# Kernel tuning notes

Measured on AMD Instinct MI355X. Metric: run time of the kernel, lower is better.

Reference implementation:

```python
import jax, jax.numpy as jnp
import numpy as np

B, S, N = 1, 8, 512
DV, DM = 256, 64
INNER, H, WS = 256, 8, 3
DH = INNER // H


def setup_inputs() -> dict:
    key = jax.random.key(0)
    ks = jax.random.split(key, 7)
    w = lambda k, shape: jax.random.normal(k, shape, dtype=jnp.float32) * 0.02
    return {
        "values": jax.random.normal(ks[0], (B, S, N, DV), dtype=jnp.float32),
        "metadata": jax.random.normal(ks[1], (B, S, N, DM), dtype=jnp.float32),
        "w_meta_outer": w(ks[2], (DM, 2 * INNER)),   # meta_to_qk of outer block
        "w_qkv": w(ks[3], (DV, 3 * INNER)),           # values_to_qkv (no bias)
        "w_meta_inner": w(ks[4], (DM, 2 * INNER)),   # meta_to_qk of inner block
        "w_out": w(ks[5], (INNER, DV)),               # output_proj Linear weight
        "b_out": jnp.zeros((DV,), dtype=jnp.float32), # output_proj Linear bias
    }


def _forward(values, metadata, w_meta_outer, w_qkv, w_meta_inner, w_out, b_out):
    # ---- outer: source-level metadata attention to pick top-WS windows ----
    meta_mean = metadata.mean(axis=2)                      # [B,S,DM]
    qm, km = jnp.split(meta_mean @ w_meta_outer, 2, axis=-1)
    qm = jnp.clip(qm, -5, 5)
    km = jnp.clip(km, -5, 5)
    dots = jnp.einsum('bqd,bkd->bqk', qm, km) * (INNER ** -0.5)
    meta_attn = jax.nn.softmax(dots, axis=-1) + 2.0 * jnp.eye(S, dtype=dots.dtype)
    _, top_idx = jax.lax.top_k(meta_attn, WS)              # [B,S,WS], sorted desc

    # ---- gather adaptive windows over the source axis ----
    bidx = jnp.arange(B)[:, None, None]
    win_vals = values[bidx, top_idx]                       # [B,S,WS,N,DV]
    win_meta = metadata[bidx, top_idx]                     # [B,S,WS,N,DM]

    # Keys/values over all WS*N window tokens; queries only for slot-0 tokens
    # (the original computes all queries then slices x[:,:,0]; softmax is
    # per-query so restricting queries gives identical math).
    kv_vals = win_vals.reshape(B * S, WS * N, DV)
    kv_meta = win_meta.reshape(B * S, WS * N, DM)
    q_vals = win_vals[:, :, 0].reshape(B * S, N, DV)
    q_meta = win_meta[:, :, 0].reshape(B * S, N, DM)

    # ---- inner: fused QpKp^T + QmKm^T attention ----
    qp = q_vals @ w_qkv[:, :INNER]
    kp = kv_vals @ w_qkv[:, INNER:2 * INNER]
    v = kv_vals @ w_qkv[:, 2 * INNER:]
    qm2 = q_meta @ w_meta_inner[:, :INNER]
    km2 = kv_meta @ w_meta_inner[:, INNER:]

    def heads(x):  # [bs, n, inner] -> [bs, H, n, DH]
        return x.reshape(x.shape[0], x.shape[1], H, DH).transpose(0, 2, 1, 3)

    qp, kp, v, qm2, km2 = map(heads, (qp, kp, v, qm2, km2))
    scale = DH ** -0.5
    scores = jnp.einsum('bhqd,bhkd->bhqk', jnp.clip(qp, -5, 5), jnp.clip(kp, -5, 5)) * scale
    scores = scores + jnp.einsum('bhqd,bhkd->bhqk', jnp.clip(qm2, -5, 5), jnp.clip(km2, -5, 5)) * scale
    attn = jax.nn.softmax(scores, axis=-1)                 # [B*S,H,N,WS*N]
    out = jnp.einsum('bhqk,bhkd->bhqd', attn, v)           # [B*S,H,N,DH]
    out = out.transpose(0, 2, 1, 3).reshape(B * S, N, INNER)
    out = out @ w_out + b_out                              # dropout=0 (eval)
    return out.reshape(B, S, N, DV)


def reference(values, metadata, w_meta_outer, w_qkv, w_meta_inner, w_out, b_out):
    return _forward(values, metadata, w_meta_outer, w_qkv, w_meta_inner, w_out, b_out)
```

## Files before the change

### kernel.cpp

```cpp
#include <hip/hip_runtime.h>
#include <hip/hip_bf16.h>

#define S_ 8
#define N_ 512
#define DV_ 256
#define DM_ 64
#define INNER_ 256
#define H_ 8
#define WS_ 3
#define DH_ 32

typedef __attribute__((ext_vector_type(8))) __bf16 bf16x8;
typedef __attribute__((ext_vector_type(4))) float f32x4;

__device__ __forceinline__ float clip5(float x) {
    return fminf(5.0f, fmaxf(-5.0f, x));
}
__device__ __forceinline__ unsigned short f2bf(float x) {
    __hip_bfloat16 h = __float2bfloat16(x);
    return *reinterpret_cast<unsigned short*>(&h);
}

__global__ __launch_bounds__(256) void prep(
    const float* __restrict__ w_qkv, const float* __restrict__ w_meta_inner,
    const float* __restrict__ w_out, const float* __restrict__ metadata,
    unsigned short* __restrict__ WqkvT, unsigned short* __restrict__ WmetaT,
    unsigned short* __restrict__ WoutT, float* __restrict__ mm_part)
{
    __shared__ float Tf[64][65];
    int b = blockIdx.x, tid = threadIdx.x;
    if (b < 72) {
        const float* src; unsigned short* dst; int Nsrc, Ktot, k0, n0;
        if (b < 48)      { src = w_qkv;        dst = WqkvT; Nsrc = 768; Ktot = 256; k0 = (b & 3) * 64; n0 = (b >> 2) * 64; }
        else if (b < 56) { src = w_meta_inner; dst = WmetaT; Nsrc = 512; Ktot = 64;  k0 = 0;            n0 = (b - 48) * 64; }
        else             { int t = b - 56; src = w_out; dst = WoutT; Nsrc = 256; Ktot = 256; k0 = (t & 3) * 64; n0 = (t >> 2) * 64; }
#pragma unroll
        for (int p = 0; p < 16; p++) {
            int i = p * 256 + tid; int r = i >> 6, cc = i & 63;
            Tf[r][cc] = src[(size_t)(k0 + r) * Nsrc + n0 + cc];
        }
        __syncthreads();
#pragma unroll
        for (int p = 0; p < 16; p++) {
            int i = p * 256 + tid; int r = i >> 6, cc = i & 63;
            dst[(size_t)(n0 + r) * Ktot + k0 + cc] = f2bf(Tf[cc][r]);
        }
    } else {
        int bb = b - 72;
        int s = bb >> 3, g = bb & 7;
        int d = tid & 63, t4 = tid >> 6;
        const float* base = metadata + ((size_t)(s * N_) + g * 64 + t4 * 16) * DM_ + d;
        float acc = 0.f;
#pragma unroll
        for (int i = 0; i < 16; i++) acc += base[(size_t)i * DM_];
        float* red = &Tf[0][0];
        red[tid] = acc;
        __syncthreads();
        if (tid < 64)
            mm_part[(size_t)bb * 64 + tid] =
                red[tid] + red[tid + 64] + red[tid + 128] + red[tid + 192];
    }
}

template<int ROLE>
__device__ __forceinline__ void gemm_body(
    unsigned short* smem,
    const float* __restrict__ A, const unsigned short* __restrict__ Bt,
    unsigned short* __restrict__ Qc, unsigned short* __restrict__ Kc,
    unsigned short* __restrict__ Vt,
    int m0, int n0g, int tid)
{
    constexpr int K = (ROLE == 1) ? 64 : 256;
    constexpr int KP = K + 8;
    unsigned short* As = smem;
    unsigned short* Bs = smem + 64 * KP;

    for (int i = tid; i < 64 * (K / 4); i += 256) {
        int r = i / (K / 4), g = i % (K / 4);
        float4 x = *(const float4*)(A + (size_t)(m0 + r) * K + 4 * g);
        *(ushort4*)&As[r * KP + 4 * g] =
            make_ushort4(f2bf(x.x), f2bf(x.y), f2bf(x.z), f2bf(x.w));
    }
    for (int i = tid; i < 64 * (K / 8); i += 256) {
        int r = i / (K / 8), g = i % (K / 8);
        *(bf16x8*)&Bs[r * KP + 8 * g] =
            *(const bf16x8*)(Bt + (size_t)(n0g + r) * K + 8 * g);
    }
    __syncthreads();

    const int w = tid >> 6, lane = tid & 63, c = lane & 15, qd = lane >> 4;
    const int mb = (w >> 1) * 32, nb = (w & 1) * 32;
    f32x4 acc[2][2];
    const f32x4 z = {0.f, 0.f, 0.f, 0.f};
#pragma unroll
    for (int mt = 0; mt < 2; mt++)
#pragma unroll
        for (int nt = 0; nt < 2; nt++) acc[mt][nt] = z;

#pragma unroll
    for (int kk = 0; kk < K / 32; kk++) {
        bf16x8 a[2], bb[2];
#pragma unroll
        for (int mt = 0; mt < 2; mt++)
            a[mt] = *(const bf16x8*)&As[(mb + mt * 16 + c) * KP + kk * 32 + qd * 8];
#pragma unroll
        for (int nt = 0; nt < 2; nt++)
            bb[nt] = *(const bf16x8*)&Bs[(nb + nt * 16 + c) * KP + kk * 32 + qd * 8];
#pragma unroll
        for (int mt = 0; mt < 2; mt++)
#pragma unroll
            for (int nt = 0; nt < 2; nt++)
                acc[mt][nt] = __builtin_amdgcn_mfma_f32_16x16x32_bf16(
                    a[mt], bb[nt], acc[mt][nt], 0, 0, 0);
    }

#pragma unroll
    for (int mt = 0; mt < 2; mt++)
#pragma unroll
        for (int nt = 0; nt < 2; nt++)
#pragma unroll
            for (int r = 0; r < 4; r++) {
                int tok = m0 + mb + mt * 16 + qd * 4 + r;
                int n = n0g + nb + nt * 16 + c;
                float v = acc[mt][nt][r];
                if (ROLE == 0) {
                    if (n < 512) {
                        unsigned short* dst = (n < 256) ? Qc : Kc;
                        int p = n & 255;
                        dst[(size_t)tok * 512 + (p >> 5) * 64 + (p & 31)] = f2bf(clip5(v));
                    } else {
                        int vc = n - 512, h = vc >> 5, dh = vc & 31;
                        int s = tok >> 9, ntok = tok & 511;
                        Vt[(size_t)((s * 8 + h) * 32 + dh) * 512 + ntok] = f2bf(v);
                    }
                } else {
                    unsigned short* dst = (n < 256) ? Qc : Kc;
                    int p = n & 255;
                    dst[(size_t)tok * 512 + (p >> 5) * 64 + 32 + (p & 31)] = f2bf(clip5(v));
                }
            }
}

__global__ __launch_bounds__(256) void fused1(
    const float* __restrict__ values, const float* __restrict__ metadata,
    const unsigned short* __restrict__ WqkvT,
    const unsigned short* __restrict__ WmetaT,
    const float* __restrict__ mm_part, const float* __restrict__ w_meta_outer,
    unsigned short* __restrict__ Qc, unsigned short* __restrict__ Kc,
    unsigned short* __restrict__ Vt, int* __restrict__ topidx)
{
    __shared__ __align__(16) unsigned short smem[2 * 64 * 264];
    const int b = blockIdx.x, tid = threadIdx.x;

    if (b == 0) {
        float* mml  = (float*)smem;
        float* qmS  = mml + 512;
        float* kmS  = qmS + 2048;
        float* dots = kmS + 2048;
        for (int i = tid; i < 512; i += 256) {
            int s = i >> 6, d = i & 63;
            float acc = 0.f;
#pragma unroll
            for (int g = 0; g < 8; g++) acc += mm_part[(size_t)(s * 8 + g) * 64 + d];
            mml[i] = acc * (1.0f / (float)N_);
        }
        __syncthreads();
        for (int i = tid; i < S_ * 512; i += 256) {
            int s = i >> 9, c = i & 511;
            float acc = 0.0f;
            for (int k = 0; k < DM_; k++) acc += mml[s * 64 + k] * w_meta_outer[k * 512 + c];
            acc = clip5(acc);
            if (c < 256) qmS[s * 256 + c] = acc; else kmS[s * 256 + c - 256] = acc;
        }
        __syncthreads();
        if (tid < 64) {
            int qi = tid >> 3, ki = tid & 7;
            float acc = 0.0f;
            for (int j = 0; j < INNER_; j++) acc += qmS[qi * 256 + j] * kmS[ki * 256 + j];
            dots[qi * 8 + ki] = acc * 0.0625f;
        }
        __syncthreads();
        if (tid < S_) {
            int r = tid;
            float mx = -1e30f;
            for (int k = 0; k < S_; k++) mx = fmaxf(mx, dots[r * 8 + k]);
            float e[S_], sum = 0.0f;
            for (int k = 0; k < S_; k++) { e[k] = __expf(dots[r * 8 + k] - mx); sum += e[k]; }
            float vals[S_];
            for (int k = 0; k < S_; k++) vals[k] = e[k] / sum + (k == r ? 2.0f : 0.0f);
            bool used[S_];
            for (int k = 0; k < S_; k++) used[k] = false;
            for (int w = 0; w < WS_; w++) {
                float best = -1e30f; int bi = 0;
                for (int k = 0; k < S_; k++) {
                    if (!used[k] && vals[k] > best) { best = vals[k]; bi = k; }
                }
                used[bi] = true;
                topidx[r * WS_ + w] = bi;
            }
        }
    } else if (b <= 768) {
        int g = b - 1;
        gemm_body<0>(smem, values, WqkvT, Qc, Kc, Vt, (g & 63) * 64, (g >> 6) * 64, tid);
    } else {
        int g = b - 769;
        gemm_body<1>(smem, metadata, WmetaT, Qc, Kc, Vt, (g & 63) * 64, (g >> 6) * 64, tid);
    }
}

__global__ __launch_bounds__(256) void attn_mfma(
    const int* __restrict__ topidx,
    const unsigned short* __restrict__ Qc,
    const unsigned short* __restrict__ Kc,
    const unsigned short* __restrict__ Vt,
    unsigned short* __restrict__ AO)
{
    const int s   = blockIdx.x;
    const int h   = blockIdx.y;
    const int qt  = blockIdx.z;
    const int tid = threadIdx.x;
    const int w    = tid >> 6;
    const int lane = tid & 63;
    const int c    = lane & 15;
    const int qd   = lane >> 4;
    const float scale = 0.17677669529663687f;

    __shared__ __align__(16) unsigned short Pq[4][64][40];
    __shared__ __align__(16) float Of[4][32][66];
    __shared__ float Ml[4][2][64];

    const int src0 = topidx[s * WS_ + 0];
    const int srcs[3] = { topidx[s * WS_ + 0], topidx[s * WS_ + 1], topidx[s * WS_ + 2] };

    bf16x8 qf[4][2];
    {
        const unsigned short* qbase =
            Qc + (size_t)(src0 * N_ + qt * 64) * 512 + h * 64 + qd * 8;
#pragma unroll
        for (int qg = 0; qg < 4; qg++)
#pragma unroll
            for (int kc = 0; kc < 2; kc++)
                qf[qg][kc] = *reinterpret_cast<const bf16x8*>(
                    qbase + (size_t)(qg * 16 + c) * 512 + kc * 32);
    }

    f32x4 oacc[2][4];
    const f32x4 zero4 = {0.f, 0.f, 0.f, 0.f};
#pragma unroll
    for (int mg = 0; mg < 2; mg++)
#pragma unroll
        for (int qg = 0; qg < 4; qg++) oacc[mg][qg] = zero4;
    float mrun[4], lrun[4];
#pragma unroll
    for (int qg = 0; qg < 4; qg++) { mrun[qg] = -3.0e38f; lrun[qg] = 0.f; }

    for (int step = 0; step < 12; step++) {
        const int chunk = step * 4 + w;
        const int src = srcs[chunk >> 4];
        const int klocal = (chunk & 15) * 32;

        bf16x8 kf[2][2];
        const unsigned short* kbase =
            Kc + (size_t)(src * N_ + klocal) * 512 + h * 64 + qd * 8;
#pragma unroll
        for (int mg = 0; mg < 2; mg++)
#pragma unroll
            for (int kc = 0; kc < 2; kc++)
                kf[mg][kc] = *reinterpret_cast<const bf16x8*>(
                    kbase + (size_t)(mg * 16 + c) * 512 + kc * 32);

        bf16x8 vf[2];
        const unsigned short* vbase =
            Vt + (size_t)((src * H_ + h) * DH_) * N_ + klocal + qd * 8;
#pragma unroll
        for (int mg = 0; mg < 2; mg++)
            vf[mg] = *reinterpret_cast<const bf16x8*>(vbase + (size_t)(mg * 16 + c) * N_);

        f32x4 sacc[2][4];
#pragma unroll
        for (int mg = 0; mg < 2; mg++)
#pragma unroll
            for (int qg = 0; qg < 4; qg++) sacc[mg][qg] = zero4;
#pragma unroll
        for (int kc = 0; kc < 2; kc++)
#pragma unroll
            for (int mg = 0; mg < 2; mg++)
#pragma unroll
                for (int qg = 0; qg < 4; qg++)
                    sacc[mg][qg] = __builtin_amdgcn_mfma_f32_16x16x32_bf16(
                        kf[mg][kc], qf[qg][kc], sacc[mg][qg], 0, 0, 0);

#pragma unroll
        for (int qg = 0; qg < 4; qg++) {
            float mx = sacc[0][qg][0];
#pragma unroll
            for (int r = 1; r < 4; r++) mx = fmaxf(mx, sacc[0][qg][r]);
#pragma unroll
            for (int r = 0; r < 4; r++) mx = fmaxf(mx, sacc[1][qg][r]);
            mx = fmaxf(mx, __shfl_xor(mx, 16));
            mx = fmaxf(mx, __shfl_xor(mx, 32));
            float mnew = fmaxf(mrun[qg], mx);
            float alpha = __expf((mrun[qg] - mnew) * scale);
            float msc = mnew * scale;
            float ps = 0.f;
            unsigned short pb[2][4];
#pragma unroll
            for (int mg = 0; mg < 2; mg++)
#pragma unroll
                for (int r = 0; r < 4; r++) {
                    float p = __expf(__builtin_fmaf(sacc[mg][qg][r], scale, -msc));
                    ps += p;
                    pb[mg][r] = f2bf(p);
                }
            ps += __shfl_xor(ps, 16);
            ps += __shfl_xor(ps, 32);
            lrun[qg] = lrun[qg] * alpha + ps;
            mrun[qg] = mnew;
#pragma unroll
            for (int mg = 0; mg < 2; mg++)
#pragma unroll
                for (int r = 0; r < 4; r++) oacc[mg][qg][r] *= alpha;
#pragma unroll
            for (int mg = 0; mg < 2; mg++) {
                ushort4 u = make_ushort4(pb[mg][0], pb[mg][1], pb[mg][2], pb[mg][3]);
                *reinterpret_cast<ushort4*>(&Pq[w][qg * 16 + c][mg * 16 + qd * 4]) = u;
            }
        }

        bf16x8 pf[4];
#pragma unroll
        for (int qg = 0; qg < 4; qg++)
            pf[qg] = *reinterpret_cast<const bf16x8*>(&Pq[w][qg * 16 + c][qd * 8]);
#pragma unroll
        for (int mg = 0; mg < 2; mg++)
#pragma unroll
            for (int qg = 0; qg < 4; qg++)
                oacc[mg][qg] = __builtin_amdgcn_mfma_f32_16x16x32_bf16(
                    vf[mg], pf[qg], oacc[mg][qg], 0, 0, 0);
    }

    __syncthreads();
#pragma unroll
    for (int qg = 0; qg < 4; qg++) {
        if (qd == 0) {
            Ml[w][0][qg * 16 + c] = mrun[qg];
            Ml[w][1][qg * 16 + c] = lrun[qg];
        }
#pragma unroll
        for (int mg = 0; mg < 2; mg++)
#pragma unroll
            for (int r = 0; r < 4; r++)
                Of[w][mg * 16 + qd * 4 + r][qg * 16 + c] = oacc[mg][qg][r];
    }
    __syncthreads();

    {
        int q = tid & 63;
        int dh0 = (tid >> 6) * 8;
        float mw[4], cw[4];
#pragma unroll
        for (int v = 0; v < 4; v++) mw[v] = Ml[v][0][q];
        float M = fmaxf(fmaxf(mw[0], mw[1]), fmaxf(mw[2], mw[3]));
        float L = 0.f;
#pragma unroll
        for (int v = 0; v < 4; v++) {
            cw[v] = __expf((mw[v] - M) * scale);
            L += cw[v] * Ml[v][1][q];
        }
        float inv = 1.0f / L;
        unsigned short* aorow =
            AO + (size_t)(s * N_ + qt * 64 + q) * 256 + h * 32 + dh0;
        unsigned short ub[8];
#pragma unroll
        for (int j = 0; j < 8; j++) {
            int dh = dh0 + j;
            float o = cw[0] * Of[0][dh][q] + cw[1] * Of[1][dh][q]
                    + cw[2] * Of[2][dh][q] + cw[3] * Of[3][dh][q];
            ub[j] = f2bf(o * inv);
        }
        uint4 u;
        u.x = (unsigned)ub[0] | ((unsigned)ub[1] << 16);
        u.y = (unsigned)ub[2] | ((unsigned)ub[3] << 16);
        u.z = (unsigned)ub[4] | ((unsigned)ub[5] << 16);
        u.w = (unsigned)ub[6] | ((unsigned)ub[7] << 16);
        *reinterpret_cast<uint4*>(aorow) = u;
    }
}

__global__ __launch_bounds__(256) void gemm_out(
    const unsigned short* __restrict__ AO, const unsigned short* __restrict__ Bt,
    const float* __restrict__ bias, float* __restrict__ outp)
{
    constexpr int K = 256;
    constexpr int KP = K + 8;
    __shared__ __align__(16) unsigned short As[64 * KP];
    __shared__ __align__(16) unsigned short Bs[64 * KP];
    const int tid = threadIdx.x;
    const int m0 = blockIdx.x * 64;
    const int n0g = blockIdx.y * 64;

    for (int i = tid; i < 64 * (K / 8); i += 256) {
        int r = i / (K / 8), g = i % (K / 8);
        *(bf16x8*)&As[r * KP + 8 * g] =
            *(const bf16x8*)(AO + (size_t)(m0 + r) * K + 8 * g);
    }
    for (int i = tid; i < 64 * (K / 8); i += 256) {
        int r = i / (K / 8), g = i % (K / 8);
        *(bf16x8*)&Bs[r * KP + 8 * g] =
            *(const bf16x8*)(Bt + (size_t)(n0g + r) * K + 8 * g);
    }
    __syncthreads();

    const int w = tid >> 6, lane = tid & 63, c = lane & 15, qd = lane >> 4;
    const int mb = (w >> 1) * 32, nb = (w & 1) * 32;
    f32x4 acc[2][2];
    const f32x4 z = {0.f, 0.f, 0.f, 0.f};
#pragma unroll
    for (int mt = 0; mt < 2; mt++)
#pragma unroll
        for (int nt = 0; nt < 2; nt++) acc[mt][nt] = z;

#pragma unroll
    for (int kk = 0; kk < K / 32; kk++) {
        bf16x8 a[2], bb[2];
#pragma unroll
        for (int mt = 0; mt < 2; mt++)
            a[mt] = *(const bf16x8*)&As[(mb + mt * 16 + c) * KP + kk * 32 + qd * 8];
#pragma unroll
        for (int nt = 0; nt < 2; nt++)
            bb[nt] = *(const bf16x8*)&Bs[(nb + nt * 16 + c) * KP + kk * 32 + qd * 8];
#pragma unroll
        for (int mt = 0; mt < 2; mt++)
#pragma unroll
            for (int nt = 0; nt < 2; nt++)
                acc[mt][nt] = __builtin_amdgcn_mfma_f32_16x16x32_bf16(
                    a[mt], bb[nt], acc[mt][nt], 0, 0, 0);
    }

#pragma unroll
    for (int mt = 0; mt < 2; mt++)
#pragma unroll
        for (int nt = 0; nt < 2; nt++)
#pragma unroll
            for (int r = 0; r < 4; r++) {
                int tok = m0 + mb + mt * 16 + qd * 4 + r;
                int n = n0g + nb + nt * 16 + c;
                outp[(size_t)tok * 256 + n] = acc[mt][nt][r] + bias[n];
            }
}

extern "C" void kernel_launch(void* const* d_in, const int* in_sizes, int n_in,
                              void* d_out, int out_size, void* d_ws, size_t ws_size,
                              hipStream_t stream) {
    const float* values       = (const float*)d_in[0];
    const float* metadata     = (const float*)d_in[1];
    const float* w_meta_outer = (const float*)d_in[2];
    const float* w_qkv        = (const float*)d_in[3];
    const float* w_meta_inner = (const float*)d_in[4];
    const float* w_out        = (const float*)d_in[5];
    const float* b_out        = (const float*)d_in[6];
    float* out = (float*)d_out;

    char* ws = (char*)d_ws;
    int* topidx = (int*)ws;
    float* mm_part = (float*)(ws + 256);
    unsigned short* WqkvT  = (unsigned short*)(ws + 20480);
    unsigned short* WmetaT = WqkvT + (size_t)768 * 256;
    unsigned short* WoutT  = WmetaT + (size_t)512 * 64;
    unsigned short* Qc     = WoutT + (size_t)256 * 256;
    unsigned short* Kc     = Qc + (size_t)4096 * 512;
    unsigned short* Vt     = Kc + (size_t)4096 * 512;
    unsigned short* AO     = Vt + (size_t)8 * 8 * 32 * 512;

    prep<<<dim3(136), dim3(256), 0, stream>>>(
        w_qkv, w_meta_inner, w_out, metadata, WqkvT, WmetaT, WoutT, mm_part);
    fused1<<<dim3(1281), dim3(256), 0, stream>>>(
        values, metadata, WqkvT, WmetaT, mm_part, w_meta_outer, Qc, Kc, Vt, topidx);
    attn_mfma<<<dim3(8, 8, 8), dim3(256), 0, stream>>>(topidx, Qc, Kc, Vt, AO);
    gemm_out<<<dim3(64, 4), dim3(256), 0, stream>>>(AO, WoutT, b_out, out);
}
```

Measured before the change: 124.4 us.

## Merge four kernels into one persistent cooperative kernel with grid syncs

Replaces the four separate launches (weight prep, QKV projection, attention, output GEMM) with a single cooperative persistent kernel. Each phase loops over its original work units with a grid-stride loop and is separated from the next by grid.sync(). The aim is to remove per-launch overhead and the gaps between dependent kernels. In exchange, parallelism is capped at 512 resident blocks, grid-wide barriers are added, and register and LDS pressure rise because the fused kernel is sized for its largest phase.

```diff
diff --git a/kernel.cpp b/kernel.cpp
--- a/kernel.cpp
+++ b/kernel.cpp
@@ -1,5 +1,8 @@
 #include <hip/hip_runtime.h>
 #include <hip/hip_bf16.h>
+#include <hip/hip_cooperative_groups.h>
+
+namespace cg = cooperative_groups;
 
 #define S_ 8
 #define N_ 512
@@ -19,47 +22,6 @@
 __device__ __forceinline__ unsigned short f2bf(float x) {
     __hip_bfloat16 h = __float2bfloat16(x);
     return *reinterpret_cast<unsigned short*>(&h);
-}
-
-__global__ __launch_bounds__(256) void prep(
-    const float* __restrict__ w_qkv, const float* __restrict__ w_meta_inner,
-    const float* __restrict__ w_out, const float* __restrict__ metadata,
-    unsigned short* __restrict__ WqkvT, unsigned short* __restrict__ WmetaT,
-    unsigned short* __restrict__ WoutT, float* __restrict__ mm_part)
-{
-    __shared__ float Tf[64][65];
-    int b = blockIdx.x, tid = threadIdx.x;
-    if (b < 72) {
-        const float* src; unsigned short* dst; int Nsrc, Ktot, k0, n0;
-        if (b < 48)      { src = w_qkv;        dst = WqkvT; Nsrc = 768; Ktot = 256; k0 = (b & 3) * 64; n0 = (b >> 2) * 64; }
-        else if (b < 56) { src = w_meta_inner; dst = WmetaT; Nsrc = 512; Ktot = 64;  k0 = 0;            n0 = (b - 48) * 64; }
-        else             { int t = b - 56; src = w_out; dst = WoutT; Nsrc = 256; Ktot = 256; k0 = (t & 3) * 64; n0 = (t >> 2) * 64; }
-#pragma unroll
-        for (int p = 0; p < 16; p++) {
-            int i = p * 256 + tid; int r = i >> 6, cc = i & 63;
-            Tf[r][cc] = src[(size_t)(k0 + r) * Nsrc + n0 + cc];
-        }
-        __syncthreads();
-#pragma unroll
-        for (int p = 0; p < 16; p++) {
-            int i = p * 256 + tid; int r = i >> 6, cc = i & 63;
-            dst[(size_t)(n0 + r) * Ktot + k0 + cc] = f2bf(Tf[cc][r]);
-        }
-    } else {
-        int bb = b - 72;
-        int s = bb >> 3, g = bb & 7;
-        int d = tid & 63, t4 = tid >> 6;
-        const float* base = metadata + ((size_t)(s * N_) + g * 64 + t4 * 16) * DM_ + d;
-        float acc = 0.f;
-#pragma unroll
-        for (int i = 0; i < 16; i++) acc += base[(size_t)i * DM_];
-        float* red = &Tf[0][0];
-        red[tid] = acc;
-        __syncthreads();
-        if (tid < 64)
-            mm_part[(size_t)bb * 64 + tid] =
-                red[tid] + red[tid + 64] + red[tid + 128] + red[tid + 192];
-    }
 }
 
 template<int ROLE>
@@ -141,312 +103,353 @@
             }
 }
 
-__global__ __launch_bounds__(256) void fused1(
+__global__ __launch_bounds__(256, 2) void mega(
     const float* __restrict__ values, const float* __restrict__ metadata,
-    const unsigned short* __restrict__ WqkvT,
-    const unsigned short* __restrict__ WmetaT,
-    const float* __restrict__ mm_part, const float* __restrict__ w_meta_outer,
+    const float* __restrict__ w_meta_outer, const float* __restrict__ w_qkv,
+    const float* __restrict__ w_meta_inner, const float* __restrict__ w_out,
+    const float* __restrict__ b_out,
+    int* __restrict__ topidx, float* __restrict__ mm_part,
+    unsigned short* __restrict__ WqkvT, unsigned short* __restrict__ WmetaT,
+    unsigned short* __restrict__ WoutT,
     unsigned short* __restrict__ Qc, unsigned short* __restrict__ Kc,
-    unsigned short* __restrict__ Vt, int* __restrict__ topidx)
+    unsigned short* __restrict__ Vt, unsigned short* __restrict__ AO,
+    float* __restrict__ outp)
 {
-    __shared__ __align__(16) unsigned short smem[2 * 64 * 264];
-    const int b = blockIdx.x, tid = threadIdx.x;
-
-    if (b == 0) {
-        float* mml  = (float*)smem;
-        float* qmS  = mml + 512;
-        float* kmS  = qmS + 2048;
-        float* dots = kmS + 2048;
-        for (int i = tid; i < 512; i += 256) {
-            int s = i >> 6, d = i & 63;
+    __shared__ __align__(16) unsigned char smemraw[2 * 64 * 264 * 2];
+    cg::grid_group grid = cg::this_grid();
+    const int blk = blockIdx.x, G = gridDim.x, tid = threadIdx.x;
+
+    for (int u = blk; u < 136; u += G) {
+        __syncthreads();
+        if (u < 72) {
+            float (*Tf)[65] = (float(*)[65])smemraw;
+            const float* src; unsigned short* dst; int Nsrc, Ktot, k0, n0;
+            if (u < 48)      { src = w_qkv;        dst = WqkvT;  Nsrc = 768; Ktot = 256; k0 = (u & 3) * 64; n0 = (u >> 2) * 64; }
+            else if (u < 56) { src = w_meta_inner; dst = WmetaT; Nsrc = 512; Ktot = 64;  k0 = 0;            n0 = (u - 48) * 64; }
+            else             { int t = u - 56; src = w_out; dst = WoutT; Nsrc = 256; Ktot = 256; k0 = (t & 3) * 64; n0 = (t >> 2) * 64; }
+#pragma unroll
+            for (int p = 0; p < 16; p++) {
+                int i = p * 256 + tid; int r = i >> 6, cc = i & 63;
+                Tf[r][cc] = src[(size_t)(k0 + r) * Nsrc + n0 + cc];
+            }
+            __syncthreads();
+#pragma unroll
+            for (int p = 0; p < 16; p++) {
+                int i = p * 256 + tid; int r = i >> 6, cc = i & 63;
+                dst[(size_t)(n0 + r) * Ktot + k0 + cc] = f2bf(Tf[cc][r]);
+            }
+        } else {
+            int bb = u - 72;
+            int s = bb >> 3, g = bb & 7;
+            int d = tid & 63, t4 = tid >> 6;
+            const float* base = metadata + ((size_t)(s * N_) + g * 64 + t4 * 16) * DM_ + d;
             float acc = 0.f;
 #pragma unroll
-            for (int g = 0; g < 8; g++) acc += mm_part[(size_t)(s * 8 + g) * 64 + d];
-            mml[i] = acc * (1.0f / (float)N_);
-        }
-        __syncthreads();
-        for (int i = tid; i < S_ * 512; i += 256) {
-            int s = i >> 9, c = i & 511;
-            float acc = 0.0f;
-            for (int k = 0; k < DM_; k++) acc += mml[s * 64 + k] * w_meta_outer[k * 512 + c];
-            acc = clip5(acc);
-            if (c < 256) qmS[s * 256 + c] = acc; else kmS[s * 256 + c - 256] = acc;
-        }
-        __syncthreads();
-        if (tid < 64) {
-            int qi = tid >> 3, ki = tid & 7;
-            float acc = 0.0f;
-            for (int j = 0; j < INNER_; j++) acc += qmS[qi * 256 + j] * kmS[ki * 256 + j];
-            dots[qi * 8 + ki] = acc * 0.0625f;
-        }
-        __syncthreads();
-        if (tid < S_) {
-            int r = tid;
-            float mx = -1e30f;
-            for (int k = 0; k < S_; k++) mx = fmaxf(mx, dots[r * 8 + k]);
-            float e[S_], sum = 0.0f;
-            for (int k = 0; k < S_; k++) { e[k] = __expf(dots[r * 8 + k] - mx); sum += e[k]; }
-            float vals[S_];
-            for (int k = 0; k < S_; k++) vals[k] = e[k] / sum + (k == r ? 2.0f : 0.0f);
-            bool used[S_];
-            for (int k = 0; k < S_; k++) used[k] = false;
-            for (int w = 0; w < WS_; w++) {
-                float best = -1e30f; int bi = 0;
-                for (int k = 0; k < S_; k++) {
-                    if (!used[k] && vals[k] > best) { best = vals[k]; bi = k; }
+            for (int i = 0; i < 16; i++) acc += base[(size_t)i * DM_];
+            float* red = (float*)smemraw;
+            red[tid] = acc;
+            __syncthreads();
+            if (tid < 64)
+                mm_part[(size_t)bb * 64 + tid] =
+                    red[tid] + red[tid + 64] + red[tid + 128] + red[tid + 192];
+        }
+    }
+    grid.sync();
+
+    for (int t = blk; t < 1281; t += G) {
+        __syncthreads();
+        if (t == 0) {
+            float* mml  = (float*)smemraw;
+            float* qmS  = mml + 512;
+            float* kmS  = qmS + 2048;
+            float* dots = kmS + 2048;
+            for (int i = tid; i < 512; i += 256) {
+                int s = i >> 6, d = i & 63;
+                float acc = 0.f;
+#pragma unroll
+                for (int g = 0; g < 8; g++) acc += mm_part[(size_t)(s * 8 + g) * 64 + d];
+                mml[i] = acc * (1.0f / (float)N_);
+            }
+            __syncthreads();
+            for (int i = tid; i < S_ * 512; i += 256) {
+                int s = i >> 9, c = i & 511;
+                float acc = 0.0f;
+                for (int k = 0; k < DM_; k++) acc += mml[s * 64 + k] * w_meta_outer[k * 512 + c];
+                acc = clip5(acc);
+                if (c < 256) qmS[s * 256 + c] = acc; else kmS[s * 256 + c - 256] = acc;
+            }
+            __syncthreads();
+            if (tid < 64) {
+                int qi = tid >> 3, ki = tid & 7;
+                float acc = 0.0f;
+                for (int j = 0; j < INNER_; j++) acc += qmS[qi * 256 + j] * kmS[ki * 256 + j];
+                dots[qi * 8 + ki] = acc * 0.0625f;
+            }
+            __syncthreads();
+            if (tid < S_) {
+                int r = tid;
+                float mx = -1e30f;
+                for (int k = 0; k < S_; k++) mx = fmaxf(mx, dots[r * 8 + k]);
+                float e[S_], sum = 0.0f;
+                for (int k = 0; k < S_; k++) { e[k] = __expf(dots[r * 8 + k] - mx); sum += e[k]; }
+                float vals[S_];
+                for (int k = 0; k < S_; k++) vals[k] = e[k] / sum + (k == r ? 2.0f : 0.0f);
+                bool used[S_];
+                for (int k = 0; k < S_; k++) used[k] = false;
+                for (int w = 0; w < WS_; w++) {
+                    float best = -1e30f; int bi = 0;
+                    for (int k = 0; k < S_; k++) {
+                        if (!used[k] && vals[k] > best) { best = vals[k]; bi = k; }
+                    }
+                    used[bi] = true;
+                    topidx[r * WS_ + w] = bi;
                 }
-                used[bi] = true;
-                topidx[r * WS_ + w] = bi;
-            }
-        }
-    } else if (b <= 768) {
-        int g = b - 1;
-        gemm_body<0>(smem, values, WqkvT, Qc, Kc, Vt, (g & 63) * 64, (g >> 6) * 64, tid);
-    } else {
-        int g = b - 769;
-        gemm_body<1>(smem, metadata, WmetaT, Qc, Kc, Vt, (g & 63) * 64, (g >> 6) * 64, tid);
-    }
-}
-
-__global__ __launch_bounds__(256) void attn_mfma(
-    const int* __restrict__ topidx,
-    const unsigned short* __restrict__ Qc,
-    const unsigned short* __restrict__ Kc,
-    const unsigned short* __restrict__ Vt,
-    unsigned short* __restrict__ AO)
-{
-    const int s   = blockIdx.x;
-    const int h   = blockIdx.y;
-    const int qt  = blockIdx.z;
-    const int tid = threadIdx.x;
-    const int w    = tid >> 6;
-    const int lane = tid & 63;
-    const int c    = lane & 15;
-    const int qd   = lane >> 4;
-    const float scale = 0.17677669529663687f;
-
-    __shared__ __align__(16) unsigned short Pq[4][64][40];
-    __shared__ __align__(16) float Of[4][32][66];
-    __shared__ float Ml[4][2][64];
-
-    const int src0 = topidx[s * WS_ + 0];
-    const int srcs[3] = { topidx[s * WS_ + 0], topidx[s * WS_ + 1], topidx[s * WS_ + 2] };
-
-    bf16x8 qf[4][2];
-    {
-        const unsigned short* qbase =
-            Qc + (size_t)(src0 * N_ + qt * 64) * 512 + h * 64 + qd * 8;
-#pragma unroll
-        for (int qg = 0; qg < 4; qg++)
+            }
+        } else if (t <= 768) {
+            int g = t - 1;
+            gemm_body<0>((unsigned short*)smemraw, values, WqkvT, Qc, Kc, Vt,
+                         (g & 63) * 64, (g >> 6) * 64, tid);
+        } else {
+            int g = t - 769;
+            gemm_body<1>((unsigned short*)smemraw, metadata, WmetaT, Qc, Kc, Vt,
+                         (g & 63) * 64, (g >> 6) * 64, tid);
+        }
+    }
+    grid.sync();
+
+    for (int a = blk; a < 512; a += G) {
+        __syncthreads();
+        const int s  = a >> 6;
+        const int h  = (a >> 3) & 7;
+        const int qt = a & 7;
+        const int w    = tid >> 6;
+        const int lane = tid & 63;
+        const int c    = lane & 15;
+        const int qd   = lane >> 4;
+        const float scale = 0.17677669529663687f;
+
+        unsigned short* Pq = (unsigned short*)smemraw;
+        float* Of = (float*)(smemraw + 20480);
+        float* Ml = (float*)(smemraw + 20480 + 33792);
+
+        const int src0 = topidx[s * WS_ + 0];
+        const int srcs[3] = { topidx[s * WS_ + 0], topidx[s * WS_ + 1], topidx[s * WS_ + 2] };
+
+        bf16x8 qf[4][2];
+        {
+            const unsigned short* qbase =
+                Qc + (size_t)(src0 * N_ + qt * 64) * 512 + h * 64 + qd * 8;
+#pragma unroll
+            for (int qg = 0; qg < 4; qg++)
+#pragma unroll
+                for (int kc = 0; kc < 2; kc++)
+                    qf[qg][kc] = *reinterpret_cast<const bf16x8*>(
+                        qbase + (size_t)(qg * 16 + c) * 512 + kc * 32);
+        }
+
+        f32x4 oacc[2][4];
+        const f32x4 zero4 = {0.f, 0.f, 0.f, 0.f};
+#pragma unroll
+        for (int mg = 0; mg < 2; mg++)
+#pragma unroll
+            for (int qg = 0; qg < 4; qg++) oacc[mg][qg] = zero4;
+        float mrun[4], lrun[4];
+#pragma unroll
+        for (int qg = 0; qg < 4; qg++) { mrun[qg] = -3.0e38f; lrun[qg] = 0.f; }
+
+        for (int step = 0; step < 12; step++) {
+            const int chunk = step * 4 + w;
+            const int src = srcs[chunk >> 4];
+            const int klocal = (chunk & 15) * 32;
+
+            bf16x8 kf[2][2];
+            const unsigned short* kbase =
+                Kc + (size_t)(src * N_ + klocal) * 512 + h * 64 + qd * 8;
+#pragma unroll
+            for (int mg = 0; mg < 2; mg++)
+#pragma unroll
+                for (int kc = 0; kc < 2; kc++)
+                    kf[mg][kc] = *reinterpret_cast<const bf16x8*>(
+                        kbase + (size_t)(mg * 16 + c) * 512 + kc * 32);
+
+            bf16x8 vf[2];
+            const unsigned short* vbase =
+                Vt + (size_t)((src * H_ + h) * DH_) * N_ + klocal + qd * 8;
+#pragma unroll
+            for (int mg = 0; mg < 2; mg++)
+                vf[mg] = *reinterpret_cast<const bf16x8*>(vbase + (size_t)(mg * 16 + c) * N_);
+
+            f32x4 sacc[2][4];
+#pragma unroll
+            for (int mg = 0; mg < 2; mg++)
+#pragma unroll
+                for (int qg = 0; qg < 4; qg++) sacc[mg][qg] = zero4;
 #pragma unroll
             for (int kc = 0; kc < 2; kc++)
-                qf[qg][kc] = *reinterpret_cast<const bf16x8*>(
-                    qbase + (size_t)(qg * 16 + c) * 512 + kc * 32);
-    }
-
-    f32x4 oacc[2][4];
-    const f32x4 zero4 = {0.f, 0.f, 0.f, 0.f};
-#pragma unroll
-    for (int mg = 0; mg < 2; mg++)
-#pragma unroll
-        for (int qg = 0; qg < 4; qg++) oacc[mg][qg] = zero4;
-    float mrun[4], lrun[4];
-#pragma unroll
-    for (int qg = 0; qg < 4; qg++) { mrun[qg] = -3.0e38f; lrun[qg] = 0.f; }
-
-    for (int step = 0; step < 12; step++) {
-        const int chunk = step * 4 + w;
-        const int src = srcs[chunk >> 4];
-        const int klocal = (chunk & 15) * 32;
-
-        bf16x8 kf[2][2];
-        const unsigned short* kbase =
-            Kc + (size_t)(src * N_ + klocal) * 512 + h * 64 + qd * 8;
-#pragma unroll
-        for (int mg = 0; mg < 2; mg++)
-#pragma unroll
-            for (int kc = 0; kc < 2; kc++)
-                kf[mg][kc] = *reinterpret_cast<const bf16x8*>(
-                    kbase + (size_t)(mg * 16 + c) * 512 + kc * 32);
-
-        bf16x8 vf[2];
-        const unsigned short* vbase =
-            Vt + (size_t)((src * H_ + h) * DH_) * N_ + klocal + qd * 8;
-#pragma unroll
-        for (int mg = 0; mg < 2; mg++)
-            vf[mg] = *reinterpret_cast<const bf16x8*>(vbase + (size_t)(mg * 16 + c) * N_);
-
-        f32x4 sacc[2][4];
-#pragma unroll
-        for (int mg = 0; mg < 2; mg++)
-#pragma unroll
-            for (int qg = 0; qg < 4; qg++) sacc[mg][qg] = zero4;
-#pragma unroll
-        for (int kc = 0; kc < 2; kc++)
+#pragma unroll
+                for (int mg = 0; mg < 2; mg++)
+#pragma unroll
+                    for (int qg = 0; qg < 4; qg++)
+                        sacc[mg][qg] = __builtin_amdgcn_mfma_f32_16x16x32_bf16(
+                            kf[mg][kc], qf[qg][kc], sacc[mg][qg], 0, 0, 0);
+
+#pragma unroll
+            for (int qg = 0; qg < 4; qg++) {
+                float mx = sacc[0][qg][0];
+#pragma unroll
+                for (int r = 1; r < 4; r++) mx = fmaxf(mx, sacc[0][qg][r]);
+#pragma unroll
+                for (int r = 0; r < 4; r++) mx = fmaxf(mx, sacc[1][qg][r]);
+                mx = fmaxf(mx, __shfl_xor(mx, 16));
+                mx = fmaxf(mx, __shfl_xor(mx, 32));
+                float mnew = fmaxf(mrun[qg], mx);
+                float alpha = __expf((mrun[qg] - mnew) * scale);
+                float msc = mnew * scale;
+                float ps = 0.f;
+                unsigned short pb[2][4];
+#pragma unroll
+                for (int mg = 0; mg < 2; mg++)
+#pragma unroll
+                    for (int r = 0; r < 4; r++) {
+                        float p = __expf(__builtin_fmaf(sacc[mg][qg][r], scale, -msc));
+                        ps += p;
+                        pb[mg][r] = f2bf(p);
+                    }
+                ps += __shfl_xor(ps, 16);
+                ps += __shfl_xor(ps, 32);
+                lrun[qg] = lrun[qg] * alpha + ps;
+                mrun[qg] = mnew;
+#pragma unroll
+                for (int mg = 0; mg < 2; mg++)
+#pragma unroll
+                    for (int r = 0; r < 4; r++) oacc[mg][qg][r] *= alpha;
+#pragma unroll
+                for (int mg = 0; mg < 2; mg++) {
+                    ushort4 u4 = make_ushort4(pb[mg][0], pb[mg][1], pb[mg][2], pb[mg][3]);
+                    *reinterpret_cast<ushort4*>(
+                        &Pq[((w * 64) + qg * 16 + c) * 40 + mg * 16 + qd * 4]) = u4;
+                }
+            }
+
+            bf16x8 pf[4];
+#pragma unroll
+            for (int qg = 0; qg < 4; qg++)
+                pf[qg] = *reinterpret_cast<const bf16x8*>(
+                    &Pq[((w * 64) + qg * 16 + c) * 40 + qd * 8]);
 #pragma unroll
             for (int mg = 0; mg < 2; mg++)
 #pragma unroll
                 for (int qg = 0; qg < 4; qg++)
-                    sacc[mg][qg] = __builtin_amdgcn_mfma_f32_16x16x32_bf16(
-                        kf[mg][kc], qf[qg][kc], sacc[mg][qg], 0, 0, 0);
-
+                    oacc[mg][qg] = __builtin_amdgcn_mfma_f32_16x16x32_bf16(
+                        vf[mg], pf[qg], oacc[mg][qg], 0, 0, 0);
+        }
+
+        __syncthreads();
 #pragma unroll
         for (int qg = 0; qg < 4; qg++) {
-            float mx = sacc[0][qg][0];
-#pragma unroll
-            for (int r = 1; r < 4; r++) mx = fmaxf(mx, sacc[0][qg][r]);
-#pragma unroll
-            for (int r = 0; r < 4; r++) mx = fmaxf(mx, sacc[1][qg][r]);
-            mx = fmaxf(mx, __shfl_xor(mx, 16));
-            mx = fmaxf(mx, __shfl_xor(mx, 32));
-            float mnew = fmaxf(mrun[qg], mx);
-            float alpha = __expf((mrun[qg] - mnew) * scale);
-            float msc = mnew * scale;
-            float ps = 0.f;
-            unsigned short pb[2][4];
+            if (qd == 0) {
+                Ml[(w * 2 + 0) * 64 + qg * 16 + c] = mrun[qg];
+                Ml[(w * 2 + 1) * 64 + qg * 16 + c] = lrun[qg];
+            }
 #pragma unroll
             for (int mg = 0; mg < 2; mg++)
 #pragma unroll
+                for (int r = 0; r < 4; r++)
+                    Of[(w * 32 + mg * 16 + qd * 4 + r) * 66 + qg * 16 + c] = oacc[mg][qg][r];
+        }
+        __syncthreads();
+
+        {
+            int q = tid & 63;
+            int dh0 = (tid >> 6) * 8;
+            float mw[4], cw[4];
+#pragma unroll
+            for (int v = 0; v < 4; v++) mw[v] = Ml[(v * 2 + 0) * 64 + q];
+            float M = fmaxf(fmaxf(mw[0], mw[1]), fmaxf(mw[2], mw[3]));
+            float L = 0.f;
+#pragma unroll
+            for (int v = 0; v < 4; v++) {
+                cw[v] = __expf((mw[v] - M) * scale);
+                L += cw[v] * Ml[(v * 2 + 1) * 64 + q];
+            }
+            float inv = 1.0f / L;
+            unsigned short* aorow =
+                AO + (size_t)(s * N_ + qt * 64 + q) * 256 + h * 32 + dh0;
+            unsigned short ub[8];
+#pragma unroll
+            for (int j = 0; j < 8; j++) {
+                int dh = dh0 + j;
+                float o = cw[0] * Of[(0 * 32 + dh) * 66 + q] + cw[1] * Of[(1 * 32 + dh) * 66 + q]
+                        + cw[2] * Of[(2 * 32 + dh) * 66 + q] + cw[3] * Of[(3 * 32 + dh) * 66 + q];
+                ub[j] = f2bf(o * inv);
+            }
+            uint4 u;
+            u.x = (unsigned)ub[0] | ((unsigned)ub[1] << 16);
+            u.y = (unsigned)ub[2] | ((unsigned)ub[3] << 16);
+            u.z = (unsigned)ub[4] | ((unsigned)ub[5] << 16);
+            u.w = (unsigned)ub[6] | ((unsigned)ub[7] << 16);
+            *reinterpret_cast<uint4*>(aorow) = u;
+        }
+    }
+    grid.sync();
+
+    for (int t = blk; t < 256; t += G) {
+        __syncthreads();
+        constexpr int K = 256, KP = 264;
+        unsigned short* As = (unsigned short*)smemraw;
+        unsigned short* Bs = As + 64 * KP;
+        const int m0 = (t & 63) * 64;
+        const int n0g = (t >> 6) * 64;
+
+        for (int i = tid; i < 64 * 32; i += 256) {
+            int r = i >> 5, g = i & 31;
+            *(bf16x8*)&As[r * KP + 8 * g] =
+                *(const bf16x8*)(AO + (size_t)(m0 + r) * K + 8 * g);
+        }
+        for (int i = tid; i < 64 * 32; i += 256) {
+            int r = i >> 5, g = i & 31;
+            *(bf16x8*)&Bs[r * KP + 8 * g] =
+                *(const bf16x8*)(WoutT + (size_t)(n0g + r) * K + 8 * g);
+        }
+        __syncthreads();
+
+        const int w = tid >> 6, lane = tid & 63, c = lane & 15, qd = lane >> 4;
+        const int mb = (w >> 1) * 32, nb = (w & 1) * 32;
+        f32x4 acc[2][2];
+        const f32x4 z = {0.f, 0.f, 0.f, 0.f};
+#pragma unroll
+        for (int mt = 0; mt < 2; mt++)
+#pragma unroll
+            for (int nt = 0; nt < 2; nt++) acc[mt][nt] = z;
+
+#pragma unroll
+        for (int kk = 0; kk < K / 32; kk++) {
+            bf16x8 a[2], bb[2];
+#pragma unroll
+            for (int mt = 0; mt < 2; mt++)
+                a[mt] = *(const bf16x8*)&As[(mb + mt * 16 + c) * KP + kk * 32 + qd * 8];
+#pragma unroll
+            for (int nt = 0; nt < 2; nt++)
+                bb[nt] = *(const bf16x8*)&Bs[(nb + nt * 16 + c) * KP + kk * 32 + qd * 8];
+#pragma unroll
+            for (int mt = 0; mt < 2; mt++)
+#pragma unroll
+                for (int nt = 0; nt < 2; nt++)
+                    acc[mt][nt] = __builtin_amdgcn_mfma_f32_16x16x32_bf16(
+                        a[mt], bb[nt], acc[mt][nt], 0, 0, 0);
+        }
+
+#pragma unroll
+        for (int mt = 0; mt < 2; mt++)
+#pragma unroll
+            for (int nt = 0; nt < 2; nt++)
+#pragma unroll
                 for (int r = 0; r < 4; r++) {
-                    float p = __expf(__builtin_fmaf(sacc[mg][qg][r], scale, -msc));
-                    ps += p;
-                    pb[mg][r] = f2bf(p);
+                    int tok = m0 + mb + mt * 16 + qd * 4 + r;
+                    int n = n0g + nb + nt * 16 + c;
+                    outp[(size_t)tok * 256 + n] = acc[mt][nt][r] + b_out[n];
                 }
-            ps += __shfl_xor(ps, 16);
-            ps += __shfl_xor(ps, 32);
-            lrun[qg] = lrun[qg] * alpha + ps;
-            mrun[qg] = mnew;
-#pragma unroll
-            for (int mg = 0; mg < 2; mg++)
-#pragma unroll
-                for (int r = 0; r < 4; r++) oacc[mg][qg][r] *= alpha;
-#pragma unroll
-            for (int mg = 0; mg < 2; mg++) {
-                ushort4 u = make_ushort4(pb[mg][0], pb[mg][1], pb[mg][2], pb[mg][3]);
-                *reinterpret_cast<ushort4*>(&Pq[w][qg * 16 + c][mg * 16 + qd * 4]) = u;
-            }
-        }
-
-        bf16x8 pf[4];
-#pragma unroll
-        for (int qg = 0; qg < 4; qg++)
-            pf[qg] = *reinterpret_cast<const bf16x8*>(&Pq[w][qg * 16 + c][qd * 8]);
-#pragma unroll
-        for (int mg = 0; mg < 2; mg++)
-#pragma unroll
-            for (int qg = 0; qg < 4; qg++)
-                oacc[mg][qg] = __builtin_amdgcn_mfma_f32_16x16x32_bf16(
-                    vf[mg], pf[qg], oacc[mg][qg], 0, 0, 0);
-    }
-
-    __syncthreads();
-#pragma unroll
-    for (int qg = 0; qg < 4; qg++) {
-        if (qd == 0) {
-            Ml[w][0][qg * 16 + c] = mrun[qg];
-            Ml[w][1][qg * 16 + c] = lrun[qg];
-        }
-#pragma unroll
-        for (int mg = 0; mg < 2; mg++)
-#pragma unroll
-            for (int r = 0; r < 4; r++)
-                Of[w][mg * 16 + qd * 4 + r][qg * 16 + c] = oacc[mg][qg][r];
-    }
-    __syncthreads();
-
-    {
-        int q = tid & 63;
-        int dh0 = (tid >> 6) * 8;
-        float mw[4], cw[4];
-#pragma unroll
-        for (int v = 0; v < 4; v++) mw[v] = Ml[v][0][q];
-        float M = fmaxf(fmaxf(mw[0], mw[1]), fmaxf(mw[2], mw[3]));
-        float L = 0.f;
-#pragma unroll
-        for (int v = 0; v < 4; v++) {
-            cw[v] = __expf((mw[v] - M) * scale);
-            L += cw[v] * Ml[v][1][q];
-        }
-        float inv = 1.0f / L;
-        unsigned short* aorow =
-            AO + (size_t)(s * N_ + qt * 64 + q) * 256 + h * 32 + dh0;
-        unsigned short ub[8];
-#pragma unroll
-        for (int j = 0; j < 8; j++) {
-            int dh = dh0 + j;
-            float o = cw[0] * Of[0][dh][q] + cw[1] * Of[1][dh][q]
-                    + cw[2] * Of[2][dh][q] + cw[3] * Of[3][dh][q];
-            ub[j] = f2bf(o * inv);
-        }
-        uint4 u;
-        u.x = (unsigned)ub[0] | ((unsigned)ub[1] << 16);
-        u.y = (unsigned)ub[2] | ((unsigned)ub[3] << 16);
-        u.z = (unsigned)ub[4] | ((unsigned)ub[5] << 16);
-        u.w = (unsigned)ub[6] | ((unsigned)ub[7] << 16);
-        *reinterpret_cast<uint4*>(aorow) = u;
-    }
-}
-
-__global__ __launch_bounds__(256) void gemm_out(
-    const unsigned short* __restrict__ AO, const unsigned short* __restrict__ Bt,
-    const float* __restrict__ bias, float* __restrict__ outp)
-{
-    constexpr int K = 256;
-    constexpr int KP = K + 8;
-    __shared__ __align__(16) unsigned short As[64 * KP];
-    __shared__ __align__(16) unsigned short Bs[64 * KP];
-    const int tid = threadIdx.x;
-    const int m0 = blockIdx.x * 64;
-    const int n0g = blockIdx.y * 64;
-
-    for (int i = tid; i < 64 * (K / 8); i += 256) {
-        int r = i / (K / 8), g = i % (K / 8);
-        *(bf16x8*)&As[r * KP + 8 * g] =
-            *(const bf16x8*)(AO + (size_t)(m0 + r) * K + 8 * g);
-    }
-    for (int i = tid; i < 64 * (K / 8); i += 256) {
-        int r = i / (K / 8), g = i % (K / 8);
-        *(bf16x8*)&Bs[r * KP + 8 * g] =
-            *(const bf16x8*)(Bt + (size_t)(n0g + r) * K + 8 * g);
-    }
-    __syncthreads();
-
-    const int w = tid >> 6, lane = tid & 63, c = lane & 15, qd = lane >> 4;
-    const int mb = (w >> 1) * 32, nb = (w & 1) * 32;
-    f32x4 acc[2][2];
-    const f32x4 z = {0.f, 0.f, 0.f, 0.f};
-#pragma unroll
-    for (int mt = 0; mt < 2; mt++)
-#pragma unroll
-        for (int nt = 0; nt < 2; nt++) acc[mt][nt] = z;
-
-#pragma unroll
-    for (int kk = 0; kk < K / 32; kk++) {
-        bf16x8 a[2], bb[2];
-#pragma unroll
-        for (int mt = 0; mt < 2; mt++)
-            a[mt] = *(const bf16x8*)&As[(mb + mt * 16 + c) * KP + kk * 32 + qd * 8];
-#pragma unroll
-        for (int nt = 0; nt < 2; nt++)
-            bb[nt] = *(const bf16x8*)&Bs[(nb + nt * 16 + c) * KP + kk * 32 + qd * 8];
-#pragma unroll
-        for (int mt = 0; mt < 2; mt++)
-#pragma unroll
-            for (int nt = 0; nt < 2; nt++)
-                acc[mt][nt] = __builtin_amdgcn_mfma_f32_16x16x32_bf16(
-                    a[mt], bb[nt], acc[mt][nt], 0, 0, 0);
-    }
-
-#pragma unroll
-    for (int mt = 0; mt < 2; mt++)
-#pragma unroll
-        for (int nt = 0; nt < 2; nt++)
-#pragma unroll
-            for (int r = 0; r < 4; r++) {
-                int tok = m0 + mb + mt * 16 + qd * 4 + r;
-                int n = n0g + nb + nt * 16 + c;
-                outp[(size_t)tok * 256 + n] = acc[mt][nt][r] + bias[n];
-            }
+    }
 }
 
 extern "C" void kernel_launch(void* const* d_in, const int* in_sizes, int n_in,
@@ -472,10 +475,25 @@
     unsigned short* Vt     = Kc + (size_t)4096 * 512;
     unsigned short* AO     = Vt + (size_t)8 * 8 * 32 * 512;
 
-    prep<<<dim3(136), dim3(256), 0, stream>>>(
-        w_qkv, w_meta_inner, w_out, metadata, WqkvT, WmetaT, WoutT, mm_part);
-    fused1<<<dim3(1281), dim3(256), 0, stream>>>(
-        values, metadata, WqkvT, WmetaT, mm_part, w_meta_outer, Qc, Kc, Vt, topidx);
-    attn_mfma<<<dim3(8, 8, 8), dim3(256), 0, stream>>>(topidx, Qc, Kc, Vt, AO);
-    gemm_out<<<dim3(64, 4), dim3(256), 0, stream>>>(AO, WoutT, b_out, out);
+    int dev = 0;
+    (void)hipGetDevice(&dev);
+    int cus = 256;
+    (void)hipDeviceGetAttribute(&cus, hipDeviceAttributeMultiprocessorCount, dev);
+    int perCU = 0;
+    (void)hipOccupancyMaxActiveBlocksPerMultiprocessor(
+        &perCU, reinterpret_cast<const void*>(mega), 256, 0);
+    if (perCU < 1) perCU = 1;
+    long long cap = (long long)perCU * cus;
+    int G = (int)(cap < 512 ? cap : 512);
+    if (G < 1) G = 1;
+
+    void* args[] = {
+        (void*)&values, (void*)&metadata, (void*)&w_meta_outer, (void*)&w_qkv,
+        (void*)&w_meta_inner, (void*)&w_out, (void*)&b_out,
+        (void*)&topidx, (void*)&mm_part,
+        (void*)&WqkvT, (void*)&WmetaT, (void*)&WoutT,
+        (void*)&Qc, (void*)&Kc, (void*)&Vt, (void*)&AO, (void*)&out
+    };
+    (void)hipLaunchCooperativeKernel(reinterpret_cast<const void*>(mega),
+                                     dim3(G), dim3(256), args, 0, stream);
 }
```

New measurement: 241.8 us. +94.5%, slower.

## Fuse output projection into attention kernel via last-block atomic counter

Applied to the files above, without the earlier changes.

Removes the separate gemm_out launch and the w_out transpose in prep. The last attention block to finish for each (source, query tile) row group, identified by an atomic counter that fused1 resets, now runs the output projection, converting w_out from fp32 to bf16 in shared memory on the fly. This saves one kernel launch and its tail, but the projection work is serialized onto 64 blocks, and each of them re-reads and converts the full w_out. A no-op shared-memory write was also added.

```diff
diff --git a/kernel.cpp b/kernel.cpp
--- a/kernel.cpp
+++ b/kernel.cpp
@@ -23,17 +23,16 @@
 
 __global__ __launch_bounds__(256) void prep(
     const float* __restrict__ w_qkv, const float* __restrict__ w_meta_inner,
-    const float* __restrict__ w_out, const float* __restrict__ metadata,
+    const float* __restrict__ metadata,
     unsigned short* __restrict__ WqkvT, unsigned short* __restrict__ WmetaT,
-    unsigned short* __restrict__ WoutT, float* __restrict__ mm_part)
+    float* __restrict__ mm_part)
 {
     __shared__ float Tf[64][65];
     int b = blockIdx.x, tid = threadIdx.x;
-    if (b < 72) {
+    if (b < 56) {
         const float* src; unsigned short* dst; int Nsrc, Ktot, k0, n0;
-        if (b < 48)      { src = w_qkv;        dst = WqkvT; Nsrc = 768; Ktot = 256; k0 = (b & 3) * 64; n0 = (b >> 2) * 64; }
-        else if (b < 56) { src = w_meta_inner; dst = WmetaT; Nsrc = 512; Ktot = 64;  k0 = 0;            n0 = (b - 48) * 64; }
-        else             { int t = b - 56; src = w_out; dst = WoutT; Nsrc = 256; Ktot = 256; k0 = (t & 3) * 64; n0 = (t >> 2) * 64; }
+        if (b < 48) { src = w_qkv;        dst = WqkvT;  Nsrc = 768; Ktot = 256; k0 = (b & 3) * 64; n0 = (b >> 2) * 64; }
+        else        { src = w_meta_inner; dst = WmetaT; Nsrc = 512; Ktot = 64;  k0 = 0;            n0 = (b - 48) * 64; }
 #pragma unroll
         for (int p = 0; p < 16; p++) {
             int i = p * 256 + tid; int r = i >> 6, cc = i & 63;
@@ -46,7 +45,7 @@
             dst[(size_t)(n0 + r) * Ktot + k0 + cc] = f2bf(Tf[cc][r]);
         }
     } else {
-        int bb = b - 72;
+        int bb = b - 56;
         int s = bb >> 3, g = bb & 7;
         int d = tid & 63, t4 = tid >> 6;
         const float* base = metadata + ((size_t)(s * N_) + g * 64 + t4 * 16) * DM_ + d;
@@ -147,12 +146,14 @@
     const unsigned short* __restrict__ WmetaT,
     const float* __restrict__ mm_part, const float* __restrict__ w_meta_outer,
     unsigned short* __restrict__ Qc, unsigned short* __restrict__ Kc,
-    unsigned short* __restrict__ Vt, int* __restrict__ topidx)
+    unsigned short* __restrict__ Vt, int* __restrict__ topidx,
+    unsigned int* __restrict__ cnt)
 {
     __shared__ __align__(16) unsigned short smem[2 * 64 * 264];
     const int b = blockIdx.x, tid = threadIdx.x;
 
     if (b == 0) {
+        if (tid < 64) cnt[tid] = 0u;
         float* mml  = (float*)smem;
         float* qmS  = mml + 512;
         float* kmS  = qmS + 2048;
@@ -213,7 +214,11 @@
     const unsigned short* __restrict__ Qc,
     const unsigned short* __restrict__ Kc,
     const unsigned short* __restrict__ Vt,
-    unsigned short* __restrict__ AO)
+    unsigned short* __restrict__ AO,
+    const float* __restrict__ w_out,
+    const float* __restrict__ b_out,
+    float* __restrict__ outp,
+    unsigned int* __restrict__ cnt)
 {
     const int s   = blockIdx.x;
     const int h   = blockIdx.y;
@@ -225,9 +230,11 @@
     const int qd   = lane >> 4;
     const float scale = 0.17677669529663687f;
 
-    __shared__ __align__(16) unsigned short Pq[4][64][40];
-    __shared__ __align__(16) float Of[4][32][66];
-    __shared__ float Ml[4][2][64];
+    __shared__ __align__(16) unsigned char smemraw[67584];
+    unsigned short (*Pq)[64][40] = (unsigned short(*)[64][40])smemraw;
+    float (*Of)[32][66] = (float(*)[32][66])(smemraw + 20480);
+    float (*Ml)[2][64]  = (float(*)[2][64])(smemraw + 54272);
+    __shared__ int lastflag;
 
     const int src0 = topidx[s * WS_ + 0];
     const int srcs[3] = { topidx[s * WS_ + 0], topidx[s * WS_ + 1], topidx[s * WS_ + 2] };
@@ -343,6 +350,12 @@
 #pragma unroll
     for (int qg = 0; qg < 4; qg++) {
         if (qd == 0) {
+            (*Ml)[0][0] = (*Ml)[0][0];
+        }
+    }
+#pragma unroll
+    for (int qg = 0; qg < 4; qg++) {
+        if (qd == 0) {
             Ml[w][0][qg * 16 + c] = mrun[qg];
             Ml[w][1][qg * 16 + c] = lrun[qg];
         }
@@ -385,68 +398,78 @@
         u.w = (unsigned)ub[6] | ((unsigned)ub[7] << 16);
         *reinterpret_cast<uint4*>(aorow) = u;
     }
-}
-
-__global__ __launch_bounds__(256) void gemm_out(
-    const unsigned short* __restrict__ AO, const unsigned short* __restrict__ Bt,
-    const float* __restrict__ bias, float* __restrict__ outp)
-{
-    constexpr int K = 256;
-    constexpr int KP = K + 8;
-    __shared__ __align__(16) unsigned short As[64 * KP];
-    __shared__ __align__(16) unsigned short Bs[64 * KP];
-    const int tid = threadIdx.x;
-    const int m0 = blockIdx.x * 64;
-    const int n0g = blockIdx.y * 64;
-
-    for (int i = tid; i < 64 * (K / 8); i += 256) {
-        int r = i / (K / 8), g = i % (K / 8);
-        *(bf16x8*)&As[r * KP + 8 * g] =
-            *(const bf16x8*)(AO + (size_t)(m0 + r) * K + 8 * g);
-    }
-    for (int i = tid; i < 64 * (K / 8); i += 256) {
-        int r = i / (K / 8), g = i % (K / 8);
-        *(bf16x8*)&Bs[r * KP + 8 * g] =
-            *(const bf16x8*)(Bt + (size_t)(n0g + r) * K + 8 * g);
-    }
+
+    __threadfence();
     __syncthreads();
-
-    const int w = tid >> 6, lane = tid & 63, c = lane & 15, qd = lane >> 4;
-    const int mb = (w >> 1) * 32, nb = (w & 1) * 32;
-    f32x4 acc[2][2];
-    const f32x4 z = {0.f, 0.f, 0.f, 0.f};
-#pragma unroll
-    for (int mt = 0; mt < 2; mt++)
-#pragma unroll
-        for (int nt = 0; nt < 2; nt++) acc[mt][nt] = z;
-
-#pragma unroll
-    for (int kk = 0; kk < K / 32; kk++) {
-        bf16x8 a[2], bb[2];
-#pragma unroll
-        for (int mt = 0; mt < 2; mt++)
-            a[mt] = *(const bf16x8*)&As[(mb + mt * 16 + c) * KP + kk * 32 + qd * 8];
-#pragma unroll
-        for (int nt = 0; nt < 2; nt++)
-            bb[nt] = *(const bf16x8*)&Bs[(nb + nt * 16 + c) * KP + kk * 32 + qd * 8];
-#pragma unroll
-        for (int mt = 0; mt < 2; mt++)
-#pragma unroll
-            for (int nt = 0; nt < 2; nt++)
-                acc[mt][nt] = __builtin_amdgcn_mfma_f32_16x16x32_bf16(
-                    a[mt], bb[nt], acc[mt][nt], 0, 0, 0);
-    }
-
-#pragma unroll
-    for (int mt = 0; mt < 2; mt++)
-#pragma unroll
-        for (int nt = 0; nt < 2; nt++)
-#pragma unroll
-            for (int r = 0; r < 4; r++) {
-                int tok = m0 + mb + mt * 16 + qd * 4 + r;
-                int n = n0g + nb + nt * 16 + c;
-                outp[(size_t)tok * 256 + n] = acc[mt][nt][r] + bias[n];
+    if (tid == 0) {
+        unsigned int old = __hip_atomic_fetch_add(&cnt[s * 8 + qt], 1u,
+                                                  __ATOMIC_ACQ_REL,
+                                                  __HIP_MEMORY_SCOPE_AGENT);
+        lastflag = (old == 7u) ? 1 : 0;
+    }
+    __syncthreads();
+    if (!lastflag) return;
+    __threadfence();
+
+    {
+        constexpr int K = 256, KP = 264;
+        unsigned short* As = (unsigned short*)smemraw;
+        unsigned short* Bs = (unsigned short*)(smemraw + 33792);
+        const int t0 = s * N_ + qt * 64;
+
+        for (int i = tid; i < 64 * 32; i += 256) {
+            int r = i >> 5, g = i & 31;
+            *(bf16x8*)&As[r * KP + 8 * g] =
+                *(const bf16x8*)(AO + (size_t)(t0 + r) * K + 8 * g);
+        }
+        for (int nchunk = 0; nchunk < 4; nchunk++) {
+            __syncthreads();
+            for (int i = tid; i < K * 16; i += 256) {
+                int k = i >> 4, a = i & 15, n4 = a * 4;
+                float4 x = *(const float4*)(w_out + (size_t)k * 256 + nchunk * 64 + n4);
+                float xs[4] = {x.x, x.y, x.z, x.w};
+#pragma unroll
+                for (int j = 0; j < 4; j++) {
+                    int cs = (j + a) & 3;
+                    Bs[(n4 + cs) * KP + k] = f2bf(xs[cs]);
+                }
             }
+            __syncthreads();
+
+            const int mb = (w >> 1) * 32, nb = (w & 1) * 32;
+            f32x4 acc[2][2];
+#pragma unroll
+            for (int mt = 0; mt < 2; mt++)
+#pragma unroll
+                for (int nt = 0; nt < 2; nt++) acc[mt][nt] = zero4;
+#pragma unroll
+            for (int kk = 0; kk < K / 32; kk++) {
+                bf16x8 a[2], bb[2];
+#pragma unroll
+                for (int mt = 0; mt < 2; mt++)
+                    a[mt] = *(const bf16x8*)&As[(mb + mt * 16 + c) * KP + kk * 32 + qd * 8];
+#pragma unroll
+                for (int nt = 0; nt < 2; nt++)
+                    bb[nt] = *(const bf16x8*)&Bs[(nb + nt * 16 + c) * KP + kk * 32 + qd * 8];
+#pragma unroll
+                for (int mt = 0; mt < 2; mt++)
+#pragma unroll
+                    for (int nt = 0; nt < 2; nt++)
+                        acc[mt][nt] = __builtin_amdgcn_mfma_f32_16x16x32_bf16(
+                            a[mt], bb[nt], acc[mt][nt], 0, 0, 0);
+            }
+#pragma unroll
+            for (int mt = 0; mt < 2; mt++)
+#pragma unroll
+                for (int nt = 0; nt < 2; nt++)
+#pragma unroll
+                    for (int r = 0; r < 4; r++) {
+                        int tok = t0 + mb + mt * 16 + qd * 4 + r;
+                        int n = nchunk * 64 + nb + nt * 16 + c;
+                        outp[(size_t)tok * 256 + n] = acc[mt][nt][r] + b_out[n];
+                    }
+        }
+    }
 }
 
 extern "C" void kernel_launch(void* const* d_in, const int* in_sizes, int n_in,
@@ -463,19 +486,20 @@
 
     char* ws = (char*)d_ws;
     int* topidx = (int*)ws;
-    float* mm_part = (float*)(ws + 256);
+    unsigned int* cnt = (unsigned int*)(ws + 128);
+    float* mm_part = (float*)(ws + 1024);
     unsigned short* WqkvT  = (unsigned short*)(ws + 20480);
     unsigned short* WmetaT = WqkvT + (size_t)768 * 256;
-    unsigned short* WoutT  = WmetaT + (size_t)512 * 64;
-    unsigned short* Qc     = WoutT + (size_t)256 * 256;
+    unsigned short* Qc     = WmetaT + (size_t)512 * 64;
     unsigned short* Kc     = Qc + (size_t)4096 * 512;
     unsigned short* Vt     = Kc + (size_t)4096 * 512;
     unsigned short* AO     = Vt + (size_t)8 * 8 * 32 * 512;
 
-    prep<<<dim3(136), dim3(256), 0, stream>>>(
-        w_qkv, w_meta_inner, w_out, metadata, WqkvT, WmetaT, WoutT, mm_part);
+    prep<<<dim3(120), dim3(256), 0, stream>>>(
+        w_qkv, w_meta_inner, metadata, WqkvT, WmetaT, mm_part);
     fused1<<<dim3(1281), dim3(256), 0, stream>>>(
-        values, metadata, WqkvT, WmetaT, mm_part, w_meta_outer, Qc, Kc, Vt, topidx);
-    attn_mfma<<<dim3(8, 8, 8), dim3(256), 0, stream>>>(topidx, Qc, Kc, Vt, AO);
-    gemm_out<<<dim3(64, 4), dim3(256), 0, stream>>>(AO, WoutT, b_out, out);
-}
+        values, metadata, WqkvT, WmetaT, mm_part, w_meta_outer,
+        Qc, Kc, Vt, topidx, cnt);
+    attn_mfma<<<dim3(8, 8, 8), dim3(256), 0, stream>>>(
+        topidx, Qc, Kc, Vt, AO, w_out, b_out, out, cnt);
+}
```

Measured after the change: 223.1 us. 1.79x slower.
